# Kernel optimization log

Measured on AMD Instinct MI355X. Metric: run time of the kernel, lower is better.

Reference implementation:

```python
import jax, jax.numpy as jnp
import numpy as np

N = 100_000      # nodes
E = 3_200_000    # edges (avg degree 32)
F_IN = 37        # NCI1 num_features
H = 16           # hidden
C = 2            # NCI1 num_classes


def setup_inputs() -> dict:
    key = jax.random.key(0)
    k = jax.random.split(key, 7)
    x = jax.random.normal(k[0], (N, F_IN), dtype=jnp.float32)
    edge_index = jax.random.randint(k[1], (2, E), 0, N, dtype=jnp.int32)
    edge_weight = jax.random.uniform(k[2], (E,), dtype=jnp.float32)
    # Glorot-ish init for the two GCN linear weights, zero bias (PyG default)
    W1 = jax.random.normal(k[3], (F_IN, H), dtype=jnp.float32) * (1.0 / np.sqrt(F_IN))
    b1 = jnp.zeros((H,), dtype=jnp.float32)
    W2 = jax.random.normal(k[4], (H, C), dtype=jnp.float32) * (1.0 / np.sqrt(H))
    b2 = jnp.zeros((C,), dtype=jnp.float32)
    return {"x": x, "edge_index": edge_index, "edge_weight": edge_weight,
            "W1": W1, "b1": b1, "W2": W2, "b2": b2}


def _gcn_norm(edge_index, edge_weight, dtype):
    # PyG gcn_norm: add self-loops (weight 1.0), symmetric D^-1/2 A D^-1/2
    loop = jnp.arange(N, dtype=edge_index.dtype)
    row = jnp.concatenate([edge_index[0], loop])  # source
    col = jnp.concatenate([edge_index[1], loop])  # target (aggregation index)
    w = jnp.concatenate([edge_weight, jnp.ones((N,), dtype=dtype)])
    deg = jax.ops.segment_sum(w, col, num_segments=N)
    dinv = jnp.where(deg > 0, jax.lax.rsqrt(deg), 0.0).astype(dtype)
    norm = dinv[row] * w * dinv[col]  # [E+N]
    return row, col, norm


def _gcn_layer(x, row, col, norm, W, b):
    h = x @ W                                   # small dense transform first
    msg = norm[:, None] * h[row]                # gather + scale, [E+N, out]
    out = jax.ops.segment_sum(msg, col, num_segments=N)  # scatter-add
    return out + b


def reference(x, edge_index, edge_weight, W1, b1, W2, b2):
    row, col, norm = _gcn_norm(edge_index, edge_weight, x.dtype)
    h = jax.nn.relu(_gcn_layer(x, row, col, norm, W1, b1))
    # F.dropout with training=False is identity (module evaluated in eval mode)
    h = _gcn_layer(h, row, col, norm, W2, b2)
    return jax.nn.log_softmax(h, axis=1)
```

## Files before the change

kernel.cpp:

```cpp
#include <hip/hip_runtime.h>
#include <math.h>

#define N_NODES 100000
#define N_EDGES 3200000
#define F_IN    37
#define H_DIM   16
#define C_DIM   2

#define BUCKET_BITS 7
#define BUCKET_SZ   128
#define NBUCK       782
#define CAP         4736
#define NPBLK       512
#define EB          6250
#define EPT_P       7
#define EPT_S       5
#define NPAGE       782
#define EBUF_SLOTS  (NBUCK * CAP + EB)

__device__ __forceinline__ unsigned bf16rne(float f) {
    unsigned u = __float_as_uint(f);
    return (u + 0x7FFFu + ((u >> 16) & 1u)) >> 16;
}
__device__ __forceinline__ int2 ldnt_i2(const int2* p) {
    long long v = __builtin_nontemporal_load((const long long*)p);
    return *(int2*)&v;
}
#define BLO(u) __uint_as_float((u) << 16)
#define BHI(u) __uint_as_float((u) & 0xFFFF0000u)
#define EW(u)  __uint_as_float(((u) >> 17) << 16)
#define ER(u)  ((u) & 0x1FFFFu)

__global__ __launch_bounds__(1024) void k_part(
    const int* __restrict__ row, const int* __restrict__ col,
    const float* __restrict__ w, int* __restrict__ gcur, int2* __restrict__ ebuf)
{
    __shared__ int  cnt[NBUCK];
    __shared__ int  base[NBUCK];
    __shared__ int  gbase[NBUCK];
    __shared__ int  wscan[16];
    __shared__ unsigned short pg2b[NPAGE];
    __shared__ int2 stage[EB];
    int t = threadIdx.x;
    size_t e0 = (size_t)blockIdx.x * EB;
    int bk[EPT_P], rc[EPT_P], lofs[EPT_P];
    float wv[EPT_P];

    if (t < NBUCK) cnt[t] = 0;
    __syncthreads();
#pragma unroll
    for (int k = 0; k < EPT_P; k++) {
        int i = k * 1024 + t;
        if (i < EB) {
            size_t e = e0 + i;
            int r = __builtin_nontemporal_load(&row[e]);
            int c = __builtin_nontemporal_load(&col[e]);
            wv[k] = __builtin_nontemporal_load(&w[e]);
            bk[k] = (c >> BUCKET_BITS) & 1023;
            if (bk[k] >= NBUCK) bk[k] = NBUCK - 1;
            rc[k] = (r & 0x1FFFF) | ((c & (BUCKET_SZ - 1)) << 17);
            lofs[k] = atomicAdd(&cnt[bk[k]], 1);
        } else bk[k] = -1;
    }
    __syncthreads();
    {
        int lane = t & 63, wid = t >> 6;
        int v = (t < NBUCK) ? cnt[t] : 0;
#pragma unroll
        for (int d = 1; d < 64; d <<= 1) {
            int u = __shfl_up(v, d);
            if (lane >= d) v += u;
        }
        if (lane == 63) wscan[wid] = v;
        __syncthreads();
        if (wid == 0) {
            int u = (lane < 16) ? wscan[lane] : 0;
#pragma unroll
            for (int d = 1; d < 16; d <<= 1) {
                int u2 = __shfl_up(u, d);
                if (lane >= d) u += u2;
            }
            if (lane < 16) wscan[lane] = u;
        }
        __syncthreads();
        if (t < NBUCK) base[t] = v + ((wid > 0) ? wscan[wid - 1] : 0);
    }
    __syncthreads();
#pragma unroll
    for (int k = 0; k < EPT_P; k++) {
        if (bk[k] >= 0) {
            int pos = base[bk[k]] - cnt[bk[k]] + lofs[k];
            if (pos >= 0 && pos < EB) stage[pos] =
                make_int2(rc[k], __float_as_int(wv[k]));
        }
    }
    if (t < NBUCK) {
        int st = base[t] - cnt[t], en = base[t];
        int p0 = (st + 7) >> 3, p1 = (en - 1) >> 3;
        if (p0 < 0) p0 = 0;
        if (p1 >= NPAGE) p1 = NPAGE - 1;
        for (int p = p0; p <= p1; p++)
            pg2b[p] = (unsigned short)t;
        gbase[t] = t * CAP + atomicAdd(&gcur[t], cnt[t]);
    }
    __syncthreads();
    for (int s2 = t; s2 < EB; s2 += 1024) {
        int lo = pg2b[s2 >> 3];
        while (lo < NBUCK - 1 && base[lo] <= s2) lo++;
        int dst = gbase[lo] + (s2 - (base[lo] - cnt[lo]));
        if (dst >= 0 && dst < EBUF_SLOTS)
            ebuf[dst] = stage[s2];
    }
}

__global__ __launch_bounds__(1024) void k_sortxw1(
    const int* __restrict__ gcur, const int2* __restrict__ ebuf,
    const float* __restrict__ x, const float* __restrict__ W1,
    unsigned* __restrict__ ebuf4, int2* __restrict__ rp,
    float* __restrict__ dinv, unsigned* __restrict__ h1b)
{
    __shared__ int2  stage[CAP];
    __shared__ int   cnt[BUCKET_SZ];
    __shared__ int   base[BUCKET_SZ];
    __shared__ float sdinv[BUCKET_SZ];
    __shared__ int   wscan[16];
    __shared__ float sW[F_IN * H_DIM];
    float* xs = (float*)stage;

    int t = threadIdx.x, b = blockIdx.x;
    int s = b * CAP;
    int len = gcur[b];
    if (len > CAP) len = CAP;
    int nbase = b << BUCKET_BITS;
    if (t < BUCKET_SZ) cnt[t] = 0;
    __syncthreads();

    int2 ed[EPT_S]; int cl[EPT_S], lofs[EPT_S];
#pragma unroll
    for (int k = 0; k < EPT_S; k++) {
        int i = k * 1024 + t;
        if (i < len) {
            int2 v = ldnt_i2(&ebuf[s + i]);
            ed[k] = v;
            cl[k] = (v.x >> 17) & (BUCKET_SZ - 1);
            lofs[k] = atomicAdd(&cnt[cl[k]], 1);
        } else cl[k] = -1;
    }
    __syncthreads();
    {
        int lane = t & 63, wid = t >> 6;
        int v = (t < BUCKET_SZ) ? cnt[t] : 0;
#pragma unroll
        for (int d = 1; d < 64; d <<= 1) {
            int u = __shfl_up(v, d);
            if (lane >= d) v += u;
        }
        if (lane == 63) wscan[wid] = v;
        __syncthreads();
        if (wid == 0) {
            int u = (lane < 16) ? wscan[lane] : 0;
#pragma unroll
            for (int d = 1; d < 16; d <<= 1) {
                int u2 = __shfl_up(u, d);
                if (lane >= d) u += u2;
            }
            if (lane < 16) wscan[lane] = u;
        }
        __syncthreads();
        if (t < BUCKET_SZ) base[t] = v + ((wid > 0) ? wscan[wid - 1] : 0);
    }
    __syncthreads();
#pragma unroll
    for (int k = 0; k < EPT_S; k++) {
        if (cl[k] >= 0) {
            int pos = base[cl[k]] - cnt[cl[k]] + lofs[k];
            if (pos >= 0 && pos < CAP) stage[pos] = ed[k];
        }
    }
    __syncthreads();
    for (int i = t; i < len; i += 1024) {
        int2 v = stage[i];
        unsigned wb = bf16rne(__int_as_float(v.y));
        __builtin_nontemporal_store((wb << 17) | (unsigned)(v.x & 0x1FFFF),
                                    &ebuf4[s + i]);
    }
    {
        int n = t >> 3, l = t & 7;
        int st = base[n] - cnt[n], cn = cnt[n];
        float sum = 0.f;
        for (int i = l; i < cn; i += 8) sum += __int_as_float(stage[st + i].y);
        sum += __shfl_xor(sum, 1);
        sum += __shfl_xor(sum, 2);
        sum += __shfl_xor(sum, 4);
        if (l == 0) {
            float di = rsqrtf(sum + 1.0f);
            sdinv[n] = di;
            int c = nbase + n;
            if (c < N_NODES) {
                rp[c] = make_int2(s + st, cn);
                dinv[c] = di;
            }
        }
    }
    __syncthreads();

    for (int idx = t; idx < F_IN * H_DIM; idx += 1024) sW[idx] = W1[idx];
    {
        const float4* x4 = (const float4*)(x + (size_t)nbase * F_IN);
        const int nv4 = (BUCKET_SZ * F_IN) / 4;
        int gf0 = nbase * F_IN;
        for (int idx = t; idx < nv4; idx += 1024) {
            int gf = gf0 + 4 * idx;
            float4 v;
            if (gf + 3 < N_NODES * F_IN) {
                v = x4[idx];
            } else {
                v.x = (gf + 0 < N_NODES * F_IN) ? x[gf + 0] : 0.f;
                v.y = (gf + 1 < N_NODES * F_IN) ? x[gf + 1] : 0.f;
                v.z = (gf + 2 < N_NODES * F_IN) ? x[gf + 2] : 0.f;
                v.w = (gf + 3 < N_NODES * F_IN) ? x[gf + 3] : 0.f;
            }
            ((float4*)xs)[idx] = v;
        }
    }
    __syncthreads();
    {
        int n = t >> 3, sub = t & 7;
        int c = nbase + n;
        if (c < N_NODES) {
            const float* xi = &xs[n * F_IN];
            float a0 = 0.f, a1 = 0.f;
            for (int k = 0; k < F_IN; k++) {
                float xv = xi[k];
                a0 += xv * sW[k * H_DIM + 2 * sub];
                a1 += xv * sW[k * H_DIM + 2 * sub + 1];
            }
            float di = sdinv[n];
            unsigned pk = bf16rne(di * a0) | (bf16rne(di * a1) << 16);
            h1b[(size_t)c * 8 + sub] = pk;
        }
    }
}

__global__ __launch_bounds__(256) void k_agg1(
    const int2* __restrict__ rp, const unsigned* __restrict__ ebuf4,
    const uint4* __restrict__ h1b, const float* __restrict__ dinv,
    const float* __restrict__ b1, const float* __restrict__ W2,
    float* __restrict__ h2s)
{
    __shared__ float sW2[H_DIM * C_DIM];
    __shared__ float sb1[H_DIM];
    int t = threadIdx.x;
    if (t < H_DIM * C_DIM) sW2[t] = W2[t];
    if (t >= 32 && t < 32 + H_DIM) sb1[t - 32] = b1[t - 32];
    __syncthreads();
    int id = blockIdx.x * 256 + t;
    int c = id >> 3;
    int sub = id & 7;
    if (c >= N_NODES) return;
    int2 seg = rp[c];
    int s = seg.x, n = seg.y;
    int m = (n - sub + 7) >> 3;
    int p0i = s + sub;
    float acc[16];
#pragma unroll
    for (int j = 0; j < 16; j++) acc[j] = 0.f;

#define PROC1(u)                                                    \
    {   float a = EW(u);                                            \
        size_t rr = (size_t)ER(u) * 2;                              \
        uint4 g0 = h1b[rr];                                         \
        uint4 g1 = h1b[rr + 1];                                     \
        acc[0]  += a * BLO(g0.x); acc[1]  += a * BHI(g0.x);         \
        acc[2]  += a * BLO(g0.y); acc[3]  += a * BHI(g0.y);         \
        acc[4]  += a * BLO(g0.z); acc[5]  += a * BHI(g0.z);         \
        acc[6]  += a * BLO(g0.w); acc[7]  += a * BHI(g0.w);         \
        acc[8]  += a * BLO(g1.x); acc[9]  += a * BHI(g1.x);         \
        acc[10] += a * BLO(g1.y); acc[11] += a * BHI(g1.y);         \
        acc[12] += a * BLO(g1.z); acc[13] += a * BHI(g1.z);         \
        acc[14] += a * BLO(g1.w); acc[15] += a * BHI(g1.w); }

    int k = 0;
    if (m >= 4) {
        unsigned e0 = __builtin_nontemporal_load(&ebuf4[p0i + 0]);
        unsigned e1 = __builtin_nontemporal_load(&ebuf4[p0i + 8]);
        unsigned e2 = __builtin_nontemporal_load(&ebuf4[p0i + 16]);
        unsigned e3 = __builtin_nontemporal_load(&ebuf4[p0i + 24]);
        for (; k + 8 <= m; k += 4) {
            unsigned f0 = __builtin_nontemporal_load(&ebuf4[p0i + 8 * (k + 4)]);
            unsigned f1 = __builtin_nontemporal_load(&ebuf4[p0i + 8 * (k + 5)]);
            unsigned f2 = __builtin_nontemporal_load(&ebuf4[p0i + 8 * (k + 6)]);
            unsigned f3 = __builtin_nontemporal_load(&ebuf4[p0i + 8 * (k + 7)]);
            PROC1(e0); PROC1(e1); PROC1(e2); PROC1(e3);
            e0 = f0; e1 = f1; e2 = f2; e3 = f3;
        }
        PROC1(e0); PROC1(e1); PROC1(e2); PROC1(e3);
        k += 4;
    }
    for (; k < m; k++) {
        unsigned u = __builtin_nontemporal_load(&ebuf4[p0i + 8 * k]);
        PROC1(u);
    }
#undef PROC1

#pragma unroll
    for (int j = 0; j < 16; j++) {
        acc[j] += __shfl_xor(acc[j], 1);
        acc[j] += __shfl_xor(acc[j], 2);
        acc[j] += __shfl_xor(acc[j], 4);
    }

    float dc = dinv[c];
    const unsigned* h1w = (const unsigned*)h1b;
    unsigned gs = h1w[(size_t)c * 8 + sub];
    float r0 = fmaxf(dc * (acc[2 * sub]     + BLO(gs)) + sb1[2 * sub],     0.f);
    float r1 = fmaxf(dc * (acc[2 * sub + 1] + BHI(gs)) + sb1[2 * sub + 1], 0.f);
    float p0 = r0 * sW2[(2 * sub) * C_DIM + 0] + r1 * sW2[(2 * sub + 1) * C_DIM + 0];
    float p1 = r0 * sW2[(2 * sub) * C_DIM + 1] + r1 * sW2[(2 * sub + 1) * C_DIM + 1];
    p0 += __shfl_xor(p0, 1); p0 += __shfl_xor(p0, 2); p0 += __shfl_xor(p0, 4);
    p1 += __shfl_xor(p1, 1); p1 += __shfl_xor(p1, 2); p1 += __shfl_xor(p1, 4);
    if (sub == 0) ((float2*)h2s)[c] = make_float2(dc * p0, dc * p1);
}

__global__ __launch_bounds__(256) void k_agg2(
    const int2* __restrict__ rp, const unsigned* __restrict__ ebuf4,
    const float* __restrict__ h2s, const float* __restrict__ dinv,
    const float* __restrict__ b2, float* __restrict__ out)
{
    int id = blockIdx.x * 256 + threadIdx.x;
    int c = id >> 3, sub = id & 7;
    if (c >= N_NODES) return;
    int2 seg = rp[c];
    int s = seg.x, n = seg.y;
    const float2* h22 = (const float2*)h2s;
    int m = (n - sub + 7) >> 3;
    int p0i = s + sub;
    float a0 = 0.f, a1 = 0.f;

#define PROC2(u)                                                    \
    {   float a = EW(u);                                            \
        float2 hv = h22[ER(u)];                                     \
        a0 += a * hv.x;  a1 += a * hv.y; }

    int k = 0;
    if (m >= 4) {
        unsigned e0 = __builtin_nontemporal_load(&ebuf4[p0i + 0]);
        unsigned e1 = __builtin_nontemporal_load(&ebuf4[p0i + 8]);
        unsigned e2 = __builtin_nontemporal_load(&ebuf4[p0i + 16]);
        unsigned e3 = __builtin_nontemporal_load(&ebuf4[p0i + 24]);
        for (; k + 8 <= m; k += 4) {
            unsigned f0 = __builtin_nontemporal_load(&ebuf4[p0i + 8 * (k + 4)]);
            unsigned f1 = __builtin_nontemporal_load(&ebuf4[p0i + 8 * (k + 5)]);
            unsigned f2 = __builtin_nontemporal_load(&ebuf4[p0i + 8 * (k + 6)]);
            unsigned f3 = __builtin_nontemporal_load(&ebuf4[p0i + 8 * (k + 7)]);
            PROC2(e0); PROC2(e1); PROC2(e2); PROC2(e3);
            e0 = f0; e1 = f1; e2 = f2; e3 = f3;
        }
        PROC2(e0); PROC2(e1); PROC2(e2); PROC2(e3);
        k += 4;
    }
    for (; k < m; k++) {
        unsigned u = __builtin_nontemporal_load(&ebuf4[p0i + 8 * k]);
        PROC2(u);
    }
#undef PROC2

    a0 += __shfl_xor(a0, 1); a0 += __shfl_xor(a0, 2); a0 += __shfl_xor(a0, 4);
    a1 += __shfl_xor(a1, 1); a1 += __shfl_xor(a1, 2); a1 += __shfl_xor(a1, 4);
    if (sub == 0) {
        float dc = dinv[c];
        float2 hc = h22[c];
        float l0 = dc * (a0 + hc.x) + b2[0];
        float l1 = dc * (a1 + hc.y) + b2[1];
        float mx = fmaxf(l0, l1);
        float lse = mx + logf(expf(l0 - mx) + expf(l1 - mx));
        ((float2*)out)[c] = make_float2(l0 - lse, l1 - lse);
    }
}

extern "C" void kernel_launch(void* const* d_in, const int* in_sizes, int n_in,
                              void* d_out, int out_size, void* d_ws, size_t ws_size,
                              hipStream_t stream) {
    const float* x  = (const float*)d_in[0];
    const int*   ei = (const int*)d_in[1];
    const float* w  = (const float*)d_in[2];
    const float* W1 = (const float*)d_in[3];
    const float* b1 = (const float*)d_in[4];
    const float* W2 = (const float*)d_in[5];
    const float* b2 = (const float*)d_in[6];
    float* out = (float*)d_out;

    const int* row = ei;
    const int* col = ei + N_EDGES;

    char* ws = (char*)d_ws;
    int*      gcur  = (int*)(ws + 0);
    int2*     rp    = (int2*)(ws + 3200);
    float*    dinv  = (float*)(ws + 803200);
    unsigned* h1b   = (unsigned*)(ws + 1203200);
    float*    h2s   = (float*)(ws + 4403200);
    unsigned* ebuf4 = (unsigned*)(ws + 5203200);
    int2*     ebuf  = (int2*)(ws + 20017408);

    hipMemsetAsync(gcur, 0, 3200, stream);
    k_part    <<<NPBLK, 1024, 0, stream>>>(row, col, w, gcur, ebuf);
    k_sortxw1 <<<NBUCK, 1024, 0, stream>>>(gcur, ebuf, x, W1, ebuf4, rp, dinv, h1b);
    k_agg1    <<<(8 * N_NODES + 255) / 256, 256, 0, stream>>>(rp, ebuf4, (const uint4*)h1b, dinv, b1, W2, h2s);
    k_agg2    <<<(8 * N_NODES + 255) / 256, 256, 0, stream>>>(rp, ebuf4, h2s, dinv, b2, out);
}
```

Measured before the change: 191.0 us.

## Replace global atomic bucket scatter with per-block sorted chunks gathered by buckets

```diff
diff --git a/kernel.cpp b/kernel.cpp
--- a/kernel.cpp
+++ b/kernel.cpp
@@ -12,11 +12,10 @@
 #define NBUCK       782
 #define CAP         4736
 #define NPBLK       512
+#define NCHUNK      512
 #define EB          6250
 #define EPT_P       7
 #define EPT_S       5
-#define NPAGE       782
-#define EBUF_SLOTS  (NBUCK * CAP + EB)
 
 __device__ __forceinline__ unsigned bf16rne(float f) {
     unsigned u = __float_as_uint(f);
@@ -33,13 +32,11 @@
 
 __global__ __launch_bounds__(1024) void k_part(
     const int* __restrict__ row, const int* __restrict__ col,
-    const float* __restrict__ w, int* __restrict__ gcur, int2* __restrict__ ebuf)
+    const float* __restrict__ w, int* __restrict__ bases, int2* __restrict__ ebuf)
 {
     __shared__ int  cnt[NBUCK];
     __shared__ int  base[NBUCK];
-    __shared__ int  gbase[NBUCK];
     __shared__ int  wscan[16];
-    __shared__ unsigned short pg2b[NPAGE];
     __shared__ int2 stage[EB];
     int t = threadIdx.x;
     size_t e0 = (size_t)blockIdx.x * EB;
@@ -94,27 +91,17 @@
                 make_int2(rc[k], __float_as_int(wv[k]));
         }
     }
-    if (t < NBUCK) {
-        int st = base[t] - cnt[t], en = base[t];
-        int p0 = (st + 7) >> 3, p1 = (en - 1) >> 3;
-        if (p0 < 0) p0 = 0;
-        if (p1 >= NPAGE) p1 = NPAGE - 1;
-        for (int p = p0; p <= p1; p++)
-            pg2b[p] = (unsigned short)t;
-        gbase[t] = t * CAP + atomicAdd(&gcur[t], cnt[t]);
-    }
-    __syncthreads();
-    for (int s2 = t; s2 < EB; s2 += 1024) {
-        int lo = pg2b[s2 >> 3];
-        while (lo < NBUCK - 1 && base[lo] <= s2) lo++;
-        int dst = gbase[lo] + (s2 - (base[lo] - cnt[lo]));
-        if (dst >= 0 && dst < EBUF_SLOTS)
-            ebuf[dst] = stage[s2];
+    if (t < NBUCK) bases[blockIdx.x * NBUCK + t] = base[t] - cnt[t];
+    __syncthreads();
+    {
+        size_t o = (size_t)blockIdx.x * EB;
+        for (int s2 = t; s2 < EB; s2 += 1024)
+            ebuf[o + s2] = stage[s2];
     }
 }
 
 __global__ __launch_bounds__(1024) void k_sortxw1(
-    const int* __restrict__ gcur, const int2* __restrict__ ebuf,
+    const int* __restrict__ bases, const int2* __restrict__ ebuf,
     const float* __restrict__ x, const float* __restrict__ W1,
     unsigned* __restrict__ ebuf4, int2* __restrict__ rp,
     float* __restrict__ dinv, unsigned* __restrict__ h1b)
@@ -125,14 +112,70 @@
     __shared__ float sdinv[BUCKET_SZ];
     __shared__ int   wscan[16];
     __shared__ float sW[F_IN * H_DIM];
+    __shared__ int   cstart[NCHUNK];
+    __shared__ int   ccount[NCHUNK];
+    __shared__ int   cbase[NCHUNK];
+    __shared__ int   slen;
     float* xs = (float*)stage;
 
-    int t = threadIdx.x, b = blockIdx.x;
+    int t = threadIdx.x, bid = blockIdx.x;
+    int xcd = bid & 7, ii = bid >> 3;
+    int b = (xcd < 6) ? xcd * 98 + ii : 588 + (xcd - 6) * 97 + ii;
     int s = b * CAP;
-    int len = gcur[b];
-    if (len > CAP) len = CAP;
     int nbase = b << BUCKET_BITS;
     if (t < BUCKET_SZ) cnt[t] = 0;
+
+    int myc = 0, vincl = 0;
+    if (t < NCHUNK) {
+        int st = bases[t * NBUCK + b];
+        int en = (b == NBUCK - 1) ? EB : bases[t * NBUCK + b + 1];
+        if (st < 0) st = 0; if (st > EB) st = EB;
+        if (en < st) en = st; if (en > EB) en = EB;
+        myc = en - st;
+        if (myc > 64) myc = 64;
+        cstart[t] = st;
+        ccount[t] = myc;
+    }
+    {
+        int lane = t & 63;
+        vincl = myc;
+#pragma unroll
+        for (int d = 1; d < 64; d <<= 1) {
+            int u = __shfl_up(vincl, d);
+            if (lane >= d) vincl += u;
+        }
+        if (t < NCHUNK && lane == 63) wscan[t >> 6] = vincl;
+    }
+    __syncthreads();
+    if (t < 64) {
+        int u = (t < 8) ? wscan[t] : 0;
+#pragma unroll
+        for (int d = 1; d < 8; d <<= 1) {
+            int u2 = __shfl_up(u, d);
+            if (t >= d) u += u2;
+        }
+        if (t < 8) wscan[t] = u;
+    }
+    __syncthreads();
+    if (t < NCHUNK) {
+        int wid = t >> 6;
+        int incl = vincl + ((wid > 0) ? wscan[wid - 1] : 0);
+        cbase[t] = incl - myc;
+        if (t == NCHUNK - 1) slen = incl;
+    }
+    __syncthreads();
+    int len = slen;
+    if (len > CAP) len = CAP;
+
+    {
+        int p = t >> 1, h = t & 1;
+        int st = cstart[p], cb = cbase[p], cc = ccount[p];
+        const int2* src = &ebuf[(size_t)p * EB + st];
+        for (int i = h; i < cc; i += 2) {
+            int pos = cb + i;
+            if (pos >= 0 && pos < CAP) stage[pos] = src[i];
+        }
+    }
     __syncthreads();
 
     int2 ed[EPT_S]; int cl[EPT_S], lofs[EPT_S];
@@ -140,7 +183,7 @@
     for (int k = 0; k < EPT_S; k++) {
         int i = k * 1024 + t;
         if (i < len) {
-            int2 v = ldnt_i2(&ebuf[s + i]);
+            int2 v = stage[i];
             ed[k] = v;
             cl[k] = (v.x >> 17) & (BUCKET_SZ - 1);
             lofs[k] = atomicAdd(&cnt[cl[k]], 1);
@@ -394,17 +437,16 @@
     const int* col = ei + N_EDGES;
 
     char* ws = (char*)d_ws;
-    int*      gcur  = (int*)(ws + 0);
-    int2*     rp    = (int2*)(ws + 3200);
-    float*    dinv  = (float*)(ws + 803200);
-    unsigned* h1b   = (unsigned*)(ws + 1203200);
-    float*    h2s   = (float*)(ws + 4403200);
-    unsigned* ebuf4 = (unsigned*)(ws + 5203200);
-    int2*     ebuf  = (int2*)(ws + 20017408);
-
-    hipMemsetAsync(gcur, 0, 3200, stream);
-    k_part    <<<NPBLK, 1024, 0, stream>>>(row, col, w, gcur, ebuf);
-    k_sortxw1 <<<NBUCK, 1024, 0, stream>>>(gcur, ebuf, x, W1, ebuf4, rp, dinv, h1b);
+    int*      bases = (int*)(ws + 0);
+    int2*     rp    = (int2*)(ws + 1600768);
+    float*    dinv  = (float*)(ws + 2400768);
+    unsigned* h1b   = (unsigned*)(ws + 2800768);
+    float*    h2s   = (float*)(ws + 6000768);
+    unsigned* ebuf4 = (unsigned*)(ws + 6800768);
+    int2*     ebuf  = (int2*)(ws + 21614976);
+
+    k_part    <<<NPBLK, 1024, 0, stream>>>(row, col, w, bases, ebuf);
+    k_sortxw1 <<<NBUCK, 1024, 0, stream>>>(bases, ebuf, x, W1, ebuf4, rp, dinv, h1b);
     k_agg1    <<<(8 * N_NODES + 255) / 256, 256, 0, stream>>>(rp, ebuf4, (const uint4*)h1b, dinv, b1, W2, h2s);
     k_agg2    <<<(8 * N_NODES + 255) / 256, 256, 0, stream>>>(rp, ebuf4, h2s, dinv, b2, out);
 }
```

After: 189.7 us. About the same (-0.7%).
